# Kernel tuning notes

Measured on AMD Instinct MI355X. Metric: run time of the kernel, lower is better.

Reference implementation:

```python
import jax, jax.numpy as jnp
import numpy as np
from functools import partial

N = 512
H, W = 324, 332
C = 120
NEAR, FAR, BG = 0.01, 100.0, 1.0


def setup_inputs() -> dict:
    key = jax.random.key(0)
    k1, k2, k3, k4, k5, k6 = jax.random.split(key, 6)
    # positions: small xy, depth z in [2, 8] so everything projects on screen
    xy = 0.5 * jax.random.normal(k1, (N, 2), dtype=jnp.float32)
    z = jax.random.uniform(k2, (N, 1), dtype=jnp.float32, minval=2.0, maxval=8.0)
    positions = jnp.concatenate([xy, z], axis=-1)  # [N,3]
    rotations = jax.random.normal(k3, (N, 4), dtype=jnp.float32)  # unused by the math
    # scales in [0.5, 4.5] pixels -> small footprints, early-break never triggers
    scales = jax.random.uniform(k4, (N, 3), dtype=jnp.float32) * 4.0 + 0.5
    opacities = jax.random.uniform(k5, (N,), dtype=jnp.float32)
    spectral_features = jax.random.uniform(k6, (N, C), dtype=jnp.float32)
    tone_mapping = jnp.ones((C,), dtype=jnp.float32)
    intrinsics = jnp.array([[300.0, 0.0, 166.0],
                            [0.0, 300.0, 162.0],
                            [0.0, 0.0, 1.0]], dtype=jnp.float32)
    extrinsics = jnp.eye(4, dtype=jnp.float32)
    return {"positions": positions, "rotations": rotations, "scales": scales,
            "opacities": opacities, "spectral_features": spectral_features,
            "tone_mapping": tone_mapping, "intrinsics": intrinsics,
            "extrinsics": extrinsics}


def _render(positions, scales, opacities, spectral_features, tone_mapping,
            intrinsics, extrinsics):
    # --- projection (world -> camera -> screen) ---
    ph = jnp.concatenate([positions, jnp.ones_like(positions[:, :1])], axis=-1)  # [N,4]
    cam = ph @ extrinsics.T                     # [N,4]
    cam3 = cam[:, :3]
    proj = cam3 @ intrinsics.T                  # [N,3]
    screen = proj[:, :2] / (proj[:, 2:3] + 1e-6)  # [N,2] (x, y)
    depths = cam3[:, 2]                         # [N]

    # --- frustum / screen culling mask (kept as a validity flag) ---
    valid = (depths > NEAR) & (depths < FAR)
    valid &= (screen[:, 0] > -100.0) & (screen[:, 0] < W + 100.0)
    valid &= (screen[:, 1] > -100.0) & (screen[:, 1] < H + 100.0)

    # --- 2D covariance: diag(scale_x^2, scale_y^2), regularized inverse ---
    s2 = scales[:, :2] ** 2
    cov = jnp.zeros((positions.shape[0], 2, 2), dtype=positions.dtype)
    cov = cov.at[:, 0, 0].set(s2[:, 0]).at[:, 1, 1].set(s2[:, 1])
    cov_inv = jnp.linalg.inv(cov + 1e-4 * jnp.eye(2, dtype=positions.dtype))  # [N,2,2]

    # --- depth sort (front to back) ---
    order = jnp.argsort(depths)
    screen_s = screen[order]
    depths_s = depths[order]
    cinv_s = cov_inv[order]
    op_s = opacities[order]
    valid_s = valid[order]
    spec_s = spectral_features[order]           # [N,C]

    # pixel grid: pix[h,w] = (x=w, y=h)
    X, Y = jnp.meshgrid(jnp.arange(W), jnp.arange(H))  # each [H,W]
    pix = jnp.stack([X, Y], axis=-1).astype(positions.dtype)  # [H,W,2]

    def step(A, g):
        pos, cinv, op, v = g
        done = jnp.mean(A) > 0.99  # torch early-break condition
        off = (pos[0] < -W) | (pos[0] > 2 * W) | (pos[1] < -H) | (pos[1] > 2 * H)
        skip = done | off | jnp.logical_not(v)
        diff = pix - pos                                    # [H,W,2]
        mahal = jnp.einsum('hwi,ij,hwj->hw', diff, cinv, diff)
        alpha = op * jnp.exp(-0.5 * mahal) * (1.0 - A)      # [H,W]
        alpha = jnp.where(skip, 0.0, alpha)
        return A + alpha, alpha

    A0 = jnp.zeros((H, W), dtype=positions.dtype)
    A_final, alphas = jax.lax.scan(step, A0, (screen_s, cinv_s, op_s, valid_s))  # alphas [N,H,W]

    # spectral/depth accumulation == sum_i feature_i * alpha_i (GEMM over N)
    spectral = jnp.einsum('nc,nhw->chw', spec_s, alphas)    # [C,H,W]
    depth_img = jnp.einsum('n,nhw->hw', depths_s, alphas)   # [H,W]
    spectral = spectral + BG * (1.0 - A_final)[None]
    spectral = spectral * tone_mapping[:, None, None]
    return spectral, depth_img, A_final


def reference(positions, rotations, scales, opacities, spectral_features,
              tone_mapping, intrinsics, extrinsics):
    # rotations are accepted but unused by the original math (diagonal 2D cov)
    return _render(positions, scales, opacities, spectral_features,
                   tone_mapping, intrinsics, extrinsics)
```

## Files before the change

### kernel.cpp

```cpp
#include <hip/hip_runtime.h>
#include <math.h>

#define N_G 512
#define IMG_H 324
#define IMG_W 332
#define N_C 120
#define HW (IMG_H*IMG_W)
#define CHUNK 48
#define TSX 21
#define TSY 81
#define NT (TSX*TSY)
#define NBLK (NT*4)


__global__ __launch_bounds__(256, 4) void k_render(
    const float* __restrict__ pos, const float* __restrict__ scales,
    const float* __restrict__ opac, const float* __restrict__ Km,
    const float* __restrict__ Em, const float* __restrict__ spec,
    const float* __restrict__ tm, float* __restrict__ out)
{
  __shared__ __align__(16) float prm[N_G*8];
  __shared__ __align__(16) float buf[CHUNK*64];
  __shared__ __align__(16) float sbuf[CHUNK*32];
  __shared__ int wcnt[4];

  const int tid  = threadIdx.x;
  const int w    = tid >> 6;
  const int lane = tid & 63;
  const int tx = lane & 15, ty = lane >> 4;
  const unsigned long long ltm = (1ull << lane) - 1ull;

  const int t  = blockIdx.x >> 2;
  const int cq = blockIdx.x & 3;

  float psx[2], psy[2], pc00[2], pc11[2], pl2[2], pd[2];
  float bxmin[2], bxmax[2], bymin[2], bymax[2];
  {
    const float E0=Em[0],E1=Em[1],E2=Em[2],E3=Em[3],
                E4=Em[4],E5=Em[5],E6=Em[6],E7=Em[7],
                E8=Em[8],E9=Em[9],E10=Em[10],E11=Em[11];
    const float K0=Km[0],K1=Km[1],K2=Km[2],
                K3=Km[3],K4=Km[4],K5=Km[5],
                K6=Km[6],K7=Km[7],K8=Km[8];
    #pragma unroll
    for (int q = 0; q < 2; ++q) {
      const int g = w*128 + lane + q*64;
      float p0 = pos[g*3+0], p1 = pos[g*3+1], p2 = pos[g*3+2];
      float cam0 = E0*p0 + E1*p1 + E2*p2  + E3;
      float cam1 = E4*p0 + E5*p1 + E6*p2  + E7;
      float cam2 = E8*p0 + E9*p1 + E10*p2 + E11;
      float pr0 = K0*cam0 + K1*cam1 + K2*cam2;
      float pr1 = K3*cam0 + K4*cam1 + K5*cam2;
      float pr2 = K6*cam0 + K7*cam1 + K8*cam2;
      float inv = 1.0f/(pr2 + 1e-6f);
      float sx = pr0*inv, sy = pr1*inv;
      float depth = cam2;
      bool valid = (depth > 0.01f) && (depth < 100.0f)
                && (sx > -100.0f) && (sx < (float)IMG_W + 100.0f)
                && (sy > -100.0f) && (sy < (float)IMG_H + 100.0f);
      bool off = (sx < -(float)IMG_W) || (sx > 2.0f*(float)IMG_W)
              || (sy < -(float)IMG_H) || (sy > 2.0f*(float)IMG_H);
      bool skip = off || (!valid);
      float s0 = scales[g*3+0], s1 = scales[g*3+1];
      float v0 = s0*s0 + 1e-4f, v1 = s1*s1 + 1e-4f;
      const float HL2E = 0.72134752f;
      psx[q] = sx; psy[q] = sy;
      pc00[q] = HL2E/v0; pc11[q] = HL2E/v1;
      pl2[q] = __log2f(skip ? 0.0f : opac[g]);
      pd[q]  = depth;
      float rx = 6.0f*sqrtf(v0);
      float ry = 6.0f*sqrtf(v1);
      bxmin[q] = skip ?  1e9f : sx - rx;
      bxmax[q] = skip ? -1e9f : sx + rx;
      bymin[q] = skip ?  1e9f : sy - ry;
      bymax[q] = skip ? -1e9f : sy + ry;
    }
  }

  const int jx = t % TSX, ky = t / TSX;
  const int bx = 10 + ((jx & 1) ? ((jx+1)>>1) : -((jx+1)>>1));
  const int by = 40 + ((ky & 1) ? ((ky+1)>>1) : -((ky+1)>>1));

  const int x = bx*16 + tx;
  const int y = by*4 + ty;
  const bool inb = (x < IMG_W) && (y < IMG_H);
  const float px = (float)min(x, IMG_W-1);
  const float py = (float)min(y, IMG_H-1);
  const float wxmin = (float)(bx*16), wxmax = wxmin + 15.0f;
  const float wymin = (float)(by*4),  wymax = wymin + 3.0f;

  bool h0 = !(bxmin[0] > wxmax || bxmax[0] < wxmin ||
              bymin[0] > wymax || bymax[0] < wymin);
  bool h1 = !(bxmin[1] > wxmax || bxmax[1] < wxmin ||
              bymin[1] > wymax || bymax[1] < wymin);
  {
    float nx0 = fminf(fmaxf(psx[0], wxmin), wxmax);
    float ny0 = fminf(fmaxf(psy[0], wymin), wymax);
    float dx0 = nx0 - psx[0], dy0 = ny0 - psy[0];
    h0 = h0 && (pl2[0] - (pc00[0]*dx0*dx0 + pc11[0]*dy0*dy0) > -24.0f);
    float nx1 = fminf(fmaxf(psx[1], wxmin), wxmax);
    float ny1 = fminf(fmaxf(psy[1], wymin), wymax);
    float dx1 = nx1 - psx[1], dy1 = ny1 - psy[1];
    h1 = h1 && (pl2[1] - (pc00[1]*dx1*dx1 + pc11[1]*dy1*dy1) > -24.0f);
  }
  unsigned long long m0 = __ballot(h0), m1 = __ballot(h1);
  int c0 = __popcll(m0);
  if (lane == 0) wcnt[w] = c0 + __popcll(m1);
  __syncthreads();
  int offw = 0;
  #pragma unroll
  for (int k = 0; k < 4; ++k) if (k < w) offw += wcnt[k];
  const int nh = wcnt[0] + wcnt[1] + wcnt[2] + wcnt[3];
  const int p0 = offw + __popcll(m0 & ltm);
  const int p1 = offw + c0 + __popcll(m1 & ltm);
  if (h0) buf[p0] = pd[0];
  if (h1) buf[p1] = pd[1];
  if (tid < 4) buf[nh + tid] = 1e30f;
  __syncthreads();

  if (h0 | h1) {
    int r0 = 0, r1 = 0;
    const float d0 = pd[0], d1 = pd[1];
    for (int j = 0; j < nh; j += 4) {
      float4 k4 = *(const float4*)&buf[j];
      if (h0) {
        r0 += (k4.x < d0 || (k4.x == d0 && j+0 < p0)) ? 1 : 0;
        r0 += (k4.y < d0 || (k4.y == d0 && j+1 < p0)) ? 1 : 0;
        r0 += (k4.z < d0 || (k4.z == d0 && j+2 < p0)) ? 1 : 0;
        r0 += (k4.w < d0 || (k4.w == d0 && j+3 < p0)) ? 1 : 0;
      }
      if (h1) {
        r1 += (k4.x < d1 || (k4.x == d1 && j+0 < p1)) ? 1 : 0;
        r1 += (k4.y < d1 || (k4.y == d1 && j+1 < p1)) ? 1 : 0;
        r1 += (k4.z < d1 || (k4.z == d1 && j+2 < p1)) ? 1 : 0;
        r1 += (k4.w < d1 || (k4.w == d1 && j+3 < p1)) ? 1 : 0;
      }
    }
    if (h0) {
      *(float4*)&prm[r0*8]   = make_float4(psx[0], psy[0], pc00[0], pc11[0]);
      *(float4*)&prm[r0*8+4] = make_float4(pl2[0], pd[0],
                                 __int_as_float((w*128 + lane)*N_C), 0.0f);
    }
    if (h1) {
      *(float4*)&prm[r1*8]   = make_float4(psx[1], psy[1], pc00[1], pc11[1]);
      *(float4*)&prm[r1*8+4] = make_float4(pl2[1], pd[1],
                                 __int_as_float((w*128 + lane + 64)*N_C), 0.0f);
    }
  }
  __syncthreads();

  float T = 1.0f, dacc = 0.0f;
  float4 acc0 = {0,0,0,0}, acc1 = {0,0,0,0};
  const int g0 = cq + 8*w;
  const bool g1ok = (g0 + 4) < 30;
  const int stc = 16*(lane >> 2) + 4*cq + (lane & 3);
  const bool stok = (lane < 32) && (stc < N_C);

  for (int cb = 0; cb < nh; cb += CHUNK) {
    const int nc = min(CHUNK, nh - cb);

    #pragma unroll 2
    for (int j = w; j < nc; j += 4) {
      float4 q0 = *(const float4*)&prm[(cb+j)*8];
      float4 q1 = *(const float4*)&prm[(cb+j)*8+4];
      float dx = px - q0.x, dy = py - q0.y;
      float m = q0.z*dx*dx + q0.w*dy*dy;
      buf[j*64 + lane] = exp2f(q1.x - m);
      int sbase = __float_as_int(q1.z);
      if (stok) sbuf[j*32 + lane] = spec[sbase + stc];
    }
    __syncthreads();

    #pragma unroll 2
    for (int j = 0; j < nc; ++j) {
      float a  = buf[j*64 + lane];
      float wv = a * T;
      T *= (1.0f - a);
      if (w == 0)
        dacc = fmaf(prm[(cb+j)*8+5], wv, dacc);
      const float* row = &sbuf[j*32 + 8*w];
      float4 s0 = *(const float4*)(row);
      acc0.x = fmaf(wv, s0.x, acc0.x);
      acc0.y = fmaf(wv, s0.y, acc0.y);
      acc0.z = fmaf(wv, s0.z, acc0.z);
      acc0.w = fmaf(wv, s0.w, acc0.w);
      if (g1ok) {
        float4 s1 = *(const float4*)(row + 4);
        acc1.x = fmaf(wv, s1.x, acc1.x);
        acc1.y = fmaf(wv, s1.y, acc1.y);
        acc1.z = fmaf(wv, s1.z, acc1.z);
        acc1.w = fmaf(wv, s1.w, acc1.w);
      }
    }
    __syncthreads();
    if (!__ballot(T >= 1e-5f)) break;
  }

  if (inb) {
    const int pixi = y*IMG_W + x;
    const float bgT = T;
    float4 t0 = *(const float4*)&tm[4*g0];
    out[(4*g0+0)*HW + pixi] = (acc0.x + bgT)*t0.x;
    out[(4*g0+1)*HW + pixi] = (acc0.y + bgT)*t0.y;
    out[(4*g0+2)*HW + pixi] = (acc0.z + bgT)*t0.z;
    out[(4*g0+3)*HW + pixi] = (acc0.w + bgT)*t0.w;
    if (g1ok) {
      const int g1 = g0 + 4;
      float4 t1 = *(const float4*)&tm[4*g1];
      out[(4*g1+0)*HW + pixi] = (acc1.x + bgT)*t1.x;
      out[(4*g1+1)*HW + pixi] = (acc1.y + bgT)*t1.y;
      out[(4*g1+2)*HW + pixi] = (acc1.z + bgT)*t1.z;
      out[(4*g1+3)*HW + pixi] = (acc1.w + bgT)*t1.w;
    }
    if (cq == 2 && w == 0) out[N_C*HW + pixi] = dacc;
    if (cq == 3 && w == 0) out[N_C*HW + HW + pixi] = 1.0f - T;
  }
}

extern "C" void kernel_launch(void* const* d_in, const int* in_sizes, int n_in,
                              void* d_out, int out_size, void* d_ws, size_t ws_size,
                              hipStream_t stream) {
  const float* pos    = (const float*)d_in[0];
  const float* scales = (const float*)d_in[2];
  const float* opac   = (const float*)d_in[3];
  const float* spec   = (const float*)d_in[4];
  const float* tm     = (const float*)d_in[5];
  const float* K      = (const float*)d_in[6];
  const float* E      = (const float*)d_in[7];
  float* out = (float*)d_out;
  (void)d_ws; (void)ws_size;

  k_render<<<NBLK, 256, 0, stream>>>(pos, scales, opac, K, E, spec, tm, out);
}
```

Measured before the change: 109.8 us.

## Handle all 120 channels per tile block instead of splitting channels across four blocks

Each block previously handled one of four channel quarters, so per-tile work such as projection, culling, depth sorting and alpha computation ran four times. Now a single block per tile covers all channels: each warp accumulates up to 8 float4 channel groups and the spectral staging buffer holds full 120-channel rows, with CHUNK reduced to 32 to bound shared memory. This removes the redundant preprocessing and sort, but gives a quarter as many blocks, more accumulator registers per thread, and a longer serial accumulation loop per block.

```diff
diff --git a/kernel.cpp b/kernel.cpp
--- a/kernel.cpp
+++ b/kernel.cpp
@@ -6,11 +6,10 @@
 #define IMG_W 332
 #define N_C 120
 #define HW (IMG_H*IMG_W)
-#define CHUNK 48
+#define CHUNK 32
 #define TSX 21
 #define TSY 81
 #define NT (TSX*TSY)
-#define NBLK (NT*4)
 
 
 __global__ __launch_bounds__(256, 4) void k_render(
@@ -21,7 +20,7 @@
 {
   __shared__ __align__(16) float prm[N_G*8];
   __shared__ __align__(16) float buf[CHUNK*64];
-  __shared__ __align__(16) float sbuf[CHUNK*32];
+  __shared__ __align__(16) float sbuf[CHUNK*N_C];
   __shared__ int wcnt[4];
 
   const int tid  = threadIdx.x;
@@ -30,8 +29,7 @@
   const int tx = lane & 15, ty = lane >> 4;
   const unsigned long long ltm = (1ull << lane) - 1ull;
 
-  const int t  = blockIdx.x >> 2;
-  const int cq = blockIdx.x & 3;
+  const int t = blockIdx.x;
 
   float psx[2], psy[2], pc00[2], pc11[2], pl2[2], pd[2];
   float bxmin[2], bxmax[2], bymin[2], bymax[2];
@@ -150,11 +148,9 @@
   __syncthreads();
 
   float T = 1.0f, dacc = 0.0f;
-  float4 acc0 = {0,0,0,0}, acc1 = {0,0,0,0};
-  const int g0 = cq + 8*w;
-  const bool g1ok = (g0 + 4) < 30;
-  const int stc = 16*(lane >> 2) + 4*cq + (lane & 3);
-  const bool stok = (lane < 32) && (stc < N_C);
+  float4 acc[8] = {};
+  const int ng = (w < 2) ? 8 : 7;
+  const int cw = 4*w;
 
   for (int cb = 0; cb < nh; cb += CHUNK) {
     const int nc = min(CHUNK, nh - cb);
@@ -167,7 +163,8 @@
       float m = q0.z*dx*dx + q0.w*dy*dy;
       buf[j*64 + lane] = exp2f(q1.x - m);
       int sbase = __float_as_int(q1.z);
-      if (stok) sbuf[j*32 + lane] = spec[sbase + stc];
+      sbuf[j*N_C + lane] = spec[sbase + lane];
+      if (lane < N_C - 64) sbuf[j*N_C + 64 + lane] = spec[sbase + 64 + lane];
     }
     __syncthreads();
 
@@ -178,18 +175,16 @@
       T *= (1.0f - a);
       if (w == 0)
         dacc = fmaf(prm[(cb+j)*8+5], wv, dacc);
-      const float* row = &sbuf[j*32 + 8*w];
-      float4 s0 = *(const float4*)(row);
-      acc0.x = fmaf(wv, s0.x, acc0.x);
-      acc0.y = fmaf(wv, s0.y, acc0.y);
-      acc0.z = fmaf(wv, s0.z, acc0.z);
-      acc0.w = fmaf(wv, s0.w, acc0.w);
-      if (g1ok) {
-        float4 s1 = *(const float4*)(row + 4);
-        acc1.x = fmaf(wv, s1.x, acc1.x);
-        acc1.y = fmaf(wv, s1.y, acc1.y);
-        acc1.z = fmaf(wv, s1.z, acc1.z);
-        acc1.w = fmaf(wv, s1.w, acc1.w);
+      const float* row = &sbuf[j*N_C + cw];
+      #pragma unroll
+      for (int k = 0; k < 8; ++k) {
+        if (k < ng) {
+          float4 s4 = *(const float4*)(row + 16*k);
+          acc[k].x = fmaf(wv, s4.x, acc[k].x);
+          acc[k].y = fmaf(wv, s4.y, acc[k].y);
+          acc[k].z = fmaf(wv, s4.z, acc[k].z);
+          acc[k].w = fmaf(wv, s4.w, acc[k].w);
+        }
       }
     }
     __syncthreads();
@@ -199,21 +194,19 @@
   if (inb) {
     const int pixi = y*IMG_W + x;
     const float bgT = T;
-    float4 t0 = *(const float4*)&tm[4*g0];
-    out[(4*g0+0)*HW + pixi] = (acc0.x + bgT)*t0.x;
-    out[(4*g0+1)*HW + pixi] = (acc0.y + bgT)*t0.y;
-    out[(4*g0+2)*HW + pixi] = (acc0.z + bgT)*t0.z;
-    out[(4*g0+3)*HW + pixi] = (acc0.w + bgT)*t0.w;
-    if (g1ok) {
-      const int g1 = g0 + 4;
-      float4 t1 = *(const float4*)&tm[4*g1];
-      out[(4*g1+0)*HW + pixi] = (acc1.x + bgT)*t1.x;
-      out[(4*g1+1)*HW + pixi] = (acc1.y + bgT)*t1.y;
-      out[(4*g1+2)*HW + pixi] = (acc1.z + bgT)*t1.z;
-      out[(4*g1+3)*HW + pixi] = (acc1.w + bgT)*t1.w;
-    }
-    if (cq == 2 && w == 0) out[N_C*HW + pixi] = dacc;
-    if (cq == 3 && w == 0) out[N_C*HW + HW + pixi] = 1.0f - T;
+    #pragma unroll
+    for (int k = 0; k < 8; ++k) {
+      if (k < ng) {
+        const int c = cw + 16*k;
+        float4 t4 = *(const float4*)&tm[c];
+        out[(c+0)*HW + pixi] = (acc[k].x + bgT)*t4.x;
+        out[(c+1)*HW + pixi] = (acc[k].y + bgT)*t4.y;
+        out[(c+2)*HW + pixi] = (acc[k].z + bgT)*t4.z;
+        out[(c+3)*HW + pixi] = (acc[k].w + bgT)*t4.w;
+      }
+    }
+    if (w == 0) out[N_C*HW + pixi] = dacc;
+    if (w == 1) out[N_C*HW + HW + pixi] = 1.0f - T;
   }
 }
 
@@ -230,5 +223,5 @@
   float* out = (float*)d_out;
   (void)d_ws; (void)ws_size;
 
-  k_render<<<NBLK, 256, 0, stream>>>(pos, scales, opac, K, E, spec, tm, out);
+  k_render<<<NT, 256, 0, stream>>>(pos, scales, opac, K, E, spec, tm, out);
 }
```

Measured after the change: 118.1 us. 1.08x slower.

## Double-buffer alpha and spectral staging to overlap with compositing

Applied to the files above, without the earlier changes.

Splits the alpha and spectral shared-memory staging into two buffers and halves the chunk size. The next chunk's alphas and spectral rows are computed while the current chunk is composited, which removes one barrier per chunk and should hide global-load latency. It also changes each block's channel mapping from interleaved to contiguous 32-channel slices, so spectral loads are contiguous per gaussian. The cost is more work per chunk for gaussians past the early-termination point, plus the same total LDS footprint.

```diff
diff --git a/kernel.cpp b/kernel.cpp
--- a/kernel.cpp
+++ b/kernel.cpp
@@ -6,7 +6,7 @@
 #define IMG_W 332
 #define N_C 120
 #define HW (IMG_H*IMG_W)
-#define CHUNK 48
+#define CHUNK 24
 #define TSX 21
 #define TSY 81
 #define NT (TSX*TSY)
@@ -20,8 +20,8 @@
     const float* __restrict__ tm, float* __restrict__ out)
 {
   __shared__ __align__(16) float prm[N_G*8];
-  __shared__ __align__(16) float buf[CHUNK*64];
-  __shared__ __align__(16) float sbuf[CHUNK*32];
+  __shared__ __align__(16) float abuf[2][CHUNK*64];
+  __shared__ __align__(16) float sbuf[2][CHUNK*32];
   __shared__ int wcnt[4];
 
   const int tid  = threadIdx.x;
@@ -111,18 +111,19 @@
   #pragma unroll
   for (int k = 0; k < 4; ++k) if (k < w) offw += wcnt[k];
   const int nh = wcnt[0] + wcnt[1] + wcnt[2] + wcnt[3];
+  float* key = abuf[0];
   const int p0 = offw + __popcll(m0 & ltm);
   const int p1 = offw + c0 + __popcll(m1 & ltm);
-  if (h0) buf[p0] = pd[0];
-  if (h1) buf[p1] = pd[1];
-  if (tid < 4) buf[nh + tid] = 1e30f;
+  if (h0) key[p0] = pd[0];
+  if (h1) key[p1] = pd[1];
+  if (tid < 4) key[nh + tid] = 1e30f;
   __syncthreads();
 
   if (h0 | h1) {
     int r0 = 0, r1 = 0;
     const float d0 = pd[0], d1 = pd[1];
     for (int j = 0; j < nh; j += 4) {
-      float4 k4 = *(const float4*)&buf[j];
+      float4 k4 = *(const float4*)&key[j];
       if (h0) {
         r0 += (k4.x < d0 || (k4.x == d0 && j+0 < p0)) ? 1 : 0;
         r0 += (k4.y < d0 || (k4.y == d0 && j+1 < p0)) ? 1 : 0;
@@ -151,41 +152,58 @@
 
   float T = 1.0f, dacc = 0.0f;
   float4 acc0 = {0,0,0,0}, acc1 = {0,0,0,0};
-  const int g0 = cq + 8*w;
-  const bool g1ok = (g0 + 4) < 30;
-  const int stc = 16*(lane >> 2) + 4*cq + (lane & 3);
-  const bool stok = (lane < 32) && (stc < N_C);
-
-  for (int cb = 0; cb < nh; cb += CHUNK) {
-    const int nc = min(CHUNK, nh - cb);
-
+  const int c0ch = cq*32 + 4*w;
+  const bool g1ok = (cq < 3) || (w < 2);
+  const bool stok = lane < ((cq == 3) ? 24 : 32);
+  const int csta = cq*32;
+
+  {
+    const int nc0 = min(CHUNK, nh);
     #pragma unroll 2
-    for (int j = w; j < nc; j += 4) {
-      float4 q0 = *(const float4*)&prm[(cb+j)*8];
-      float4 q1 = *(const float4*)&prm[(cb+j)*8+4];
+    for (int j = w; j < nc0; j += 4) {
+      float4 q0 = *(const float4*)&prm[j*8];
+      float4 q1 = *(const float4*)&prm[j*8+4];
       float dx = px - q0.x, dy = py - q0.y;
-      float m = q0.z*dx*dx + q0.w*dy*dy;
-      buf[j*64 + lane] = exp2f(q1.x - m);
+      abuf[0][j*64 + lane] = exp2f(q1.x - (q0.z*dx*dx + q0.w*dy*dy));
       int sbase = __float_as_int(q1.z);
-      if (stok) sbuf[j*32 + lane] = spec[sbase + stc];
-    }
-    __syncthreads();
+      if (stok) sbuf[0][j*32 + lane] = spec[sbase + csta + lane];
+    }
+  }
+  __syncthreads();
+
+  for (int cb = 0, k = 0; cb < nh; cb += CHUNK, ++k) {
+    const int nc  = min(CHUNK, nh - cb);
+    const int cur = k & 1, nxt = cur ^ 1;
+
+    const int cb2 = cb + CHUNK;
+    if (cb2 < nh) {
+      const int nc2 = min(CHUNK, nh - cb2);
+      #pragma unroll 2
+      for (int j = w; j < nc2; j += 4) {
+        float4 q0 = *(const float4*)&prm[(cb2+j)*8];
+        float4 q1 = *(const float4*)&prm[(cb2+j)*8+4];
+        float dx = px - q0.x, dy = py - q0.y;
+        abuf[nxt][j*64 + lane] = exp2f(q1.x - (q0.z*dx*dx + q0.w*dy*dy));
+        int sbase = __float_as_int(q1.z);
+        if (stok) sbuf[nxt][j*32 + lane] = spec[sbase + csta + lane];
+      }
+    }
 
     #pragma unroll 2
     for (int j = 0; j < nc; ++j) {
-      float a  = buf[j*64 + lane];
+      float a  = abuf[cur][j*64 + lane];
       float wv = a * T;
       T *= (1.0f - a);
       if (w == 0)
         dacc = fmaf(prm[(cb+j)*8+5], wv, dacc);
-      const float* row = &sbuf[j*32 + 8*w];
+      const float* row = &sbuf[cur][j*32 + 4*w];
       float4 s0 = *(const float4*)(row);
       acc0.x = fmaf(wv, s0.x, acc0.x);
       acc0.y = fmaf(wv, s0.y, acc0.y);
       acc0.z = fmaf(wv, s0.z, acc0.z);
       acc0.w = fmaf(wv, s0.w, acc0.w);
       if (g1ok) {
-        float4 s1 = *(const float4*)(row + 4);
+        float4 s1 = *(const float4*)(row + 16);
         acc1.x = fmaf(wv, s1.x, acc1.x);
         acc1.y = fmaf(wv, s1.y, acc1.y);
         acc1.z = fmaf(wv, s1.z, acc1.z);
@@ -199,18 +217,18 @@
   if (inb) {
     const int pixi = y*IMG_W + x;
     const float bgT = T;
-    float4 t0 = *(const float4*)&tm[4*g0];
-    out[(4*g0+0)*HW + pixi] = (acc0.x + bgT)*t0.x;
-    out[(4*g0+1)*HW + pixi] = (acc0.y + bgT)*t0.y;
-    out[(4*g0+2)*HW + pixi] = (acc0.z + bgT)*t0.z;
-    out[(4*g0+3)*HW + pixi] = (acc0.w + bgT)*t0.w;
+    float4 t0 = *(const float4*)&tm[c0ch];
+    out[(c0ch+0)*HW + pixi] = (acc0.x + bgT)*t0.x;
+    out[(c0ch+1)*HW + pixi] = (acc0.y + bgT)*t0.y;
+    out[(c0ch+2)*HW + pixi] = (acc0.z + bgT)*t0.z;
+    out[(c0ch+3)*HW + pixi] = (acc0.w + bgT)*t0.w;
     if (g1ok) {
-      const int g1 = g0 + 4;
-      float4 t1 = *(const float4*)&tm[4*g1];
-      out[(4*g1+0)*HW + pixi] = (acc1.x + bgT)*t1.x;
-      out[(4*g1+1)*HW + pixi] = (acc1.y + bgT)*t1.y;
-      out[(4*g1+2)*HW + pixi] = (acc1.z + bgT)*t1.z;
-      out[(4*g1+3)*HW + pixi] = (acc1.w + bgT)*t1.w;
+      const int c1 = c0ch + 16;
+      float4 t1 = *(const float4*)&tm[c1];
+      out[(c1+0)*HW + pixi] = (acc1.x + bgT)*t1.x;
+      out[(c1+1)*HW + pixi] = (acc1.y + bgT)*t1.y;
+      out[(c1+2)*HW + pixi] = (acc1.z + bgT)*t1.z;
+      out[(c1+3)*HW + pixi] = (acc1.w + bgT)*t1.w;
     }
     if (cq == 2 && w == 0) out[N_C*HW + pixi] = dacc;
     if (cq == 3 && w == 0) out[N_C*HW + HW + pixi] = 1.0f - T;
```

Result: no change. 109.7 us (-0.1%).
